# Kernel optimization log

Hardware: AMD Instinct MI355X
Metric: run time of the kernel (lower is better)

## Reference

```python
import jax, jax.numpy as jnp
import numpy as np


def setup_inputs() -> dict:
    key = jax.random.key(0)
    ks = jax.random.split(key, 10)
    V, E, H, P = 50000, 300, 512, 3
    B, S = 64, 512
    stdv = 1.0 / np.sqrt(H)
    u = lambda k, shp: jax.random.uniform(k, shp, jnp.float32, -stdv, stdv)
    return {
        "text": jax.random.randint(ks[0], (B, S), 0, V),
        "embed_table": jax.random.normal(ks[1], (V, E), jnp.float32),
        "W_z": u(ks[2], (H + E, H)),
        "b_z": u(ks[3], (H,)),
        "W_r": u(ks[4], (H + E, H)),
        "b_r": u(ks[5], (H,)),
        "W_h": u(ks[6], (H + E, H)),
        "b_h": u(ks[7], (H,)),
        "dense_W": u(ks[8], (H, P)),
        "dense_b": u(ks[9], (P,)),
    }


def reference(text, embed_table, W_z, b_z, W_r, b_r, W_h, b_h, dense_W, dense_b):
    x = embed_table[text]  # [B, S, E]
    B = x.shape[0]
    H = W_z.shape[1]
    h0 = jnp.zeros((B, H), x.dtype)
    y0 = jnp.zeros((B, H), x.dtype)

    def step(carry, x_t):
        h, _ = carry
        hx = jnp.concatenate([h, x_t], axis=1)          # [B, H+E]
        z = jax.nn.sigmoid(hx @ W_z + b_z)              # update gate
        r = jax.nn.sigmoid(hx @ W_r + b_r)              # reset gate
        y = jnp.tanh(jnp.concatenate([r * h, x_t], axis=1) @ W_h + b_h)
        h_new = (1.0 - z) * h + z * y
        return (h_new, y), None

    (h_T, y_T), _ = jax.lax.scan(step, (h0, y0), jnp.swapaxes(x, 0, 1))
    out = y_T @ dense_W + dense_b  # dense applied to last candidate y_t
    return out
```

## Files before the change

kernel.cpp:

```cpp
#include <hip/hip_runtime.h>
#include <hip/hip_bf16.h>
#include <stdint.h>

#define B_ 64
#define S_ 512
#define E_ 300
#define H_ 512
#define NG_ 1536

__global__ __launch_bounds__(256) void k_init(unsigned* __restrict__ p) {
  int i = blockIdx.x * 256 + threadIdx.x;
  if (i < 100352) p[i] = 0u;
}

__global__ __launch_bounds__(256) void k_xproj(
    const int* __restrict__ text, const float* __restrict__ emb,
    const float* __restrict__ Wz, const float* __restrict__ Wr,
    const float* __restrict__ Wh, const float* __restrict__ bz,
    const float* __restrict__ br, const float* __restrict__ bh,
    float* __restrict__ X)
{
  __shared__ float xs[32][304];
  __shared__ int   toks[32];
  const int b  = blockIdx.x >> 4;
  const int s0 = (blockIdx.x & 15) << 5;
  const int t  = threadIdx.x;

  if (t < 32) toks[t] = text[b * S_ + s0 + t];
  __syncthreads();
  for (int r = 0; r < 32; ++r) {
    const float* er = emb + (size_t)toks[r] * E_;
    for (int e = t; e < E_; e += 256) xs[r][e] = er[e];
  }
  __syncthreads();

  const int c = t & 63;
  const int q = t >> 6;
  for (int n0 = 0; n0 < NG_; n0 += 64) {
    const int n  = n0 + c;
    const int g  = n >> 9;
    const int bc = n & 511;
    const float* Wg = (g == 0) ? Wz : (g == 1) ? Wr : Wh;
    const float* bg = (g == 0) ? bz : (g == 1) ? br : bh;
    float acc[8];
    const float bias = bg[bc];
    #pragma unroll
    for (int i = 0; i < 8; ++i) acc[i] = bias;
    for (int e = 0; e < E_; e += 4) {
      const float w0 = Wg[(size_t)(H_ + e) * H_ + bc];
      const float w1 = Wg[(size_t)(H_ + e + 1) * H_ + bc];
      const float w2 = Wg[(size_t)(H_ + e + 2) * H_ + bc];
      const float w3 = Wg[(size_t)(H_ + e + 3) * H_ + bc];
      #pragma unroll
      for (int i = 0; i < 8; ++i) {
        const float4 xv = *(const float4*)&xs[(q << 3) + i][e];
        acc[i] = fmaf(xv.w, w3, fmaf(xv.z, w2, fmaf(xv.y, w1, fmaf(xv.x, w0, acc[i]))));
      }
    }
    #pragma unroll
    for (int i = 0; i < 8; ++i) {
      const int s = s0 + (q << 3) + i;
      X[((size_t)s * B_ + b) * NG_ + n] = acc[i];
    }
  }
}

__device__ __forceinline__ unsigned ld_coh_u32(const unsigned* p) {
  return __hip_atomic_load(p, __ATOMIC_RELAXED, __HIP_MEMORY_SCOPE_AGENT);
}
__device__ __forceinline__ void st_coh_u32(unsigned* p, unsigned v) {
  __hip_atomic_store(p, v, __ATOMIC_RELAXED, __HIP_MEMORY_SCOPE_AGENT);
}
__device__ __forceinline__ void st_coh_f32(float* p, float v) {
  __hip_atomic_store(p, v, __ATOMIC_RELAXED, __HIP_MEMORY_SCOPE_AGENT);
}
__device__ __forceinline__ void stage_coh(const float* src, float (*dst)[516], int t) {
  #pragma unroll
  for (int u = 0; u < 8; ++u) {
    const int e = (t << 1) + (u << 9);
    const unsigned long long v = __hip_atomic_load(
        (const unsigned long long*)(src + e), __ATOMIC_RELAXED, __HIP_MEMORY_SCOPE_AGENT);
    *(unsigned long long*)&dst[u][t << 1] = v;
  }
}

__device__ __forceinline__ void group_barrier(unsigned* gflags, unsigned* myflag,
                                              unsigned gen) {
  __syncthreads();
  const int t = threadIdx.x;
  if (t < 64) {
    if (t == 0) st_coh_u32(myflag, gen);
    unsigned v;
    int it = 0;
    do {
      v = (t < 32) ? ld_coh_u32(gflags + t * 8) : gen;
    } while (__ballot(v < gen) && ++it < 4096);
  }
  __syncthreads();
}

__global__ __launch_bounds__(256, 1) void k_gru(
    const float* __restrict__ Wz, const float* __restrict__ Wr,
    const float* __restrict__ Wh, const float* __restrict__ X,
    float* __restrict__ hb, float* __restrict__ rb,
    float* __restrict__ yb, unsigned* __restrict__ flags)
{
  __shared__ float  WT[48][516];
  __shared__ float  hs[8][516];
  __shared__ float  zs[8][16];
  __shared__ float4 pbuf[256];

  const int t = threadIdx.x;
  const int g = blockIdx.x & 7;
  const int j = blockIdx.x >> 3;
  const int colblk = j << 4;
  const int b0 = g << 3;

  float* hbuf = hb + g * (8 * H_);
  float* rbuf = rb + g * (8 * H_);
  unsigned* gflags = flags + g * 256;
  unsigned* myflag = gflags + j * 8;

  for (int idx = t; idx < 48 * 512; idx += 256) {
    const int gc = idx >> 9;
    const int k  = idx & 511;
    const float* Wsel = (gc < 16) ? Wz : (gc < 32) ? Wr : Wh;
    WT[gc][k] = Wsel[(size_t)k * H_ + colblk + (gc & 15)];
  }

  const int og  = t & 63;
  const int ksi = t >> 6;
  const int rp  = og & 3;
  const int cp  = og >> 2;
  const int ogf   = t >> 2;
  const int ef    = t & 3;
  const int rowf  = ((ogf & 3) << 1) + (ef >> 1);
  const int gcolf = ((ogf >> 2) << 1) + (ef & 1);
  const int gatef = gcolf >> 4;
  const int cf    = gcolf & 15;
  const int og2  = t & 31;
  const int ksi2 = t >> 5;
  const int rp2  = og2 & 3;
  const int cp2  = og2 >> 2;
  const int rowf2 = (((t >> 2) & 3) << 1) + ((t & 3) >> 1);
  const int cf2   = (((t >> 2) >> 2) << 1) + (t & 1);

  const float* pf = (const float*)pbuf;
  unsigned nbar = 0;
  __syncthreads();

  for (int s = 0; s < S_; ++s) {
    stage_coh(hbuf, hs, t);
    __syncthreads();

    const float* Xs = X + ((size_t)s * B_ + b0) * NG_;
    const float xv1 = Xs[rowf * NG_ + gatef * H_ + colblk + cf];
    const float xv2 = (t < 128) ? Xs[rowf2 * NG_ + 2 * H_ + colblk + cf2] : 0.f;

    {
      float p00 = 0.f, p01 = 0.f, p10 = 0.f, p11 = 0.f;
      const float* h0 = &hs[(rp << 1) + 0][0];
      const float* h1 = &hs[(rp << 1) + 1][0];
      const float* w0 = &WT[(cp << 1) + 0][0];
      const float* w1 = &WT[(cp << 1) + 1][0];
      const int k0 = ksi << 7;
      #pragma unroll 4
      for (int k = k0; k < k0 + 128; k += 4) {
        const float4 a = *(const float4*)&h0[k];
        const float4 b = *(const float4*)&h1[k];
        const float4 u = *(const float4*)&w0[k];
        const float4 v = *(const float4*)&w1[k];
        p00 = fmaf(a.x,u.x,p00); p00 = fmaf(a.y,u.y,p00); p00 = fmaf(a.z,u.z,p00); p00 = fmaf(a.w,u.w,p00);
        p01 = fmaf(a.x,v.x,p01); p01 = fmaf(a.y,v.y,p01); p01 = fmaf(a.z,v.z,p01); p01 = fmaf(a.w,v.w,p01);
        p10 = fmaf(b.x,u.x,p10); p10 = fmaf(b.y,u.y,p10); p10 = fmaf(b.z,u.z,p10); p10 = fmaf(b.w,u.w,p10);
        p11 = fmaf(b.x,v.x,p11); p11 = fmaf(b.y,v.y,p11); p11 = fmaf(b.z,v.z,p11); p11 = fmaf(b.w,v.w,p11);
      }
      pbuf[(ksi << 6) + og] = make_float4(p00, p01, p10, p11);
    }
    __syncthreads();
    {
      const float sum = pf[t] + pf[256 + t] + pf[512 + t] + pf[768 + t];
      const float pre = sum + xv1;
      const float sig = 1.f / (1.f + __expf(-pre));
      if (gatef == 0) zs[rowf][cf] = sig;
      else st_coh_f32(&rbuf[rowf * H_ + colblk + cf],
                      sig * hs[rowf][colblk + cf]);
    }

    group_barrier(gflags, myflag, ++nbar);

    float hold = 0.f, zv = 0.f;
    if (t < 128) { hold = hs[rowf2][colblk + cf2]; zv = zs[rowf2][cf2]; }
    __syncthreads();

    stage_coh(rbuf, hs, t);
    __syncthreads();

    {
      float p00 = 0.f, p01 = 0.f, p10 = 0.f, p11 = 0.f;
      const float* h0 = &hs[(rp2 << 1) + 0][0];
      const float* h1 = &hs[(rp2 << 1) + 1][0];
      const float* w0 = &WT[32 + (cp2 << 1) + 0][0];
      const float* w1 = &WT[32 + (cp2 << 1) + 1][0];
      const int k0 = ksi2 << 6;
      #pragma unroll 4
      for (int k = k0; k < k0 + 64; k += 4) {
        const float4 a = *(const float4*)&h0[k];
        const float4 b = *(const float4*)&h1[k];
        const float4 u = *(const float4*)&w0[k];
        const float4 v = *(const float4*)&w1[k];
        p00 = fmaf(a.x,u.x,p00); p00 = fmaf(a.y,u.y,p00); p00 = fmaf(a.z,u.z,p00); p00 = fmaf(a.w,u.w,p00);
        p01 = fmaf(a.x,v.x,p01); p01 = fmaf(a.y,v.y,p01); p01 = fmaf(a.z,v.z,p01); p01 = fmaf(a.w,v.w,p01);
        p10 = fmaf(b.x,u.x,p10); p10 = fmaf(b.y,u.y,p10); p10 = fmaf(b.z,u.z,p10); p10 = fmaf(b.w,u.w,p10);
        p11 = fmaf(b.x,v.x,p11); p11 = fmaf(b.y,v.y,p11); p11 = fmaf(b.z,v.z,p11); p11 = fmaf(b.w,v.w,p11);
      }
      pbuf[(ksi2 << 5) + og2] = make_float4(p00, p01, p10, p11);
    }
    __syncthreads();
    if (t < 128) {
      float sum = pf[t];
      #pragma unroll
      for (int q = 1; q < 8; ++q) sum += pf[(q << 7) + t];
      const float pre = sum + xv2;
      const float ex  = __expf(2.f * pre);
      const float y   = (ex - 1.f) / (ex + 1.f);
      const float hnew = (1.f - zv) * hold + zv * y;
      st_coh_f32(&hbuf[rowf2 * H_ + colblk + cf2], hnew);
      if (s == S_ - 1) yb[(b0 + rowf2) * H_ + colblk + cf2] = y;
    }

    group_barrier(gflags, myflag, ++nbar);
  }
}

__global__ __launch_bounds__(256) void k_dense(
    const float* __restrict__ yb, const float* __restrict__ dW,
    const float* __restrict__ db, float* __restrict__ out)
{
  const int t = threadIdx.x;
  if (t >= 192) return;
  const int b = t / 3, p = t % 3;
  float acc = db[p];
  const float* yr = yb + b * H_;
  for (int k = 0; k < H_; ++k) acc = fmaf(yr[k], dW[k * 3 + p], acc);
  out[b * 3 + p] = acc;
}

extern "C" void kernel_launch(void* const* d_in, const int* in_sizes, int n_in,
                              void* d_out, int out_size, void* d_ws, size_t ws_size,
                              hipStream_t stream) {
  const int*   text = (const int*)d_in[0];
  const float* emb  = (const float*)d_in[1];
  const float* Wz   = (const float*)d_in[2];
  const float* bz   = (const float*)d_in[3];
  const float* Wr   = (const float*)d_in[4];
  const float* br   = (const float*)d_in[5];
  const float* Wh   = (const float*)d_in[6];
  const float* bh   = (const float*)d_in[7];
  const float* dW   = (const float*)d_in[8];
  const float* db   = (const float*)d_in[9];
  float* out = (float*)d_out;

  float*    X    = (float*)d_ws;
  float*    hbp  = (float*)((char*)d_ws + (size_t)201326592);
  float*    rbp  = hbp + 32768;
  float*    ybp  = rbp + 32768;
  unsigned* flgp = (unsigned*)(ybp + 32768);

  hipLaunchKernelGGL(k_init, dim3(392), dim3(256), 0, stream, (unsigned*)hbp);

  hipLaunchKernelGGL(k_xproj, dim3(1024), dim3(256), 0, stream,
                     text, emb, Wz, Wr, Wh, bz, br, bh, X);

  const float* Wz_ = Wz; const float* Wr_ = Wr; const float* Wh_ = Wh;
  const float* X_ = X; float* hb_ = hbp; float* rb_ = rbp; float* yb_ = ybp;
  unsigned* flg_ = flgp;
  void* kargs[] = { (void*)&Wz_, (void*)&Wr_, (void*)&Wh_, (void*)&X_,
                    (void*)&hb_, (void*)&rb_, (void*)&yb_, (void*)&flg_ };
  hipLaunchCooperativeKernel((void*)k_gru, dim3(256), dim3(256), kargs, 0, stream);

  hipLaunchKernelGGL(k_dense, dim3(1), dim3(256), 0, stream, ybp, dW, db, out);
}
```

Baseline: 7.011 ms.

## Use 4x4 register tiles in GRU step GEMV and overlap barrier with prefetch

The recurrent matvec in k_gru is restructured so each thread computes a 4x4 register tile of (row, column) outputs over a k-slice. Partial sums are reduced with wave shuffles and then across waves through a smaller pbuf, which cuts LDS traffic per FMA. The group barrier is split into a flag publish and a separate poll, so the next step's X-projection loads and the hold/z reads run while other blocks arrive. The k_xproj kernel also now computes four adjacent columns per thread using float4 weight loads and stores. The cost is more registers per thread and shuffle overhead in exchange for fewer shared-memory loads and hidden sync latency.

```diff
diff --git a/kernel.cpp b/kernel.cpp
--- a/kernel.cpp
+++ b/kernel.cpp
@@ -34,33 +34,45 @@
   }
   __syncthreads();
 
-  const int c = t & 63;
-  const int q = t >> 6;
-  for (int n0 = 0; n0 < NG_; n0 += 64) {
-    const int n  = n0 + c;
+  const int c4 = t & 63;
+  const int q  = t >> 6;
+  for (int chunk = 0; chunk < 6; ++chunk) {
+    const int n  = chunk * 256 + (c4 << 2);
     const int g  = n >> 9;
     const int bc = n & 511;
     const float* Wg = (g == 0) ? Wz : (g == 1) ? Wr : Wh;
     const float* bg = (g == 0) ? bz : (g == 1) ? br : bh;
-    float acc[8];
-    const float bias = bg[bc];
-    #pragma unroll
-    for (int i = 0; i < 8; ++i) acc[i] = bias;
+    float acc[8][4];
+    {
+      const float4 bv = *(const float4*)&bg[bc];
+      #pragma unroll
+      for (int i = 0; i < 8; ++i) {
+        acc[i][0] = bv.x; acc[i][1] = bv.y; acc[i][2] = bv.z; acc[i][3] = bv.w;
+      }
+    }
     for (int e = 0; e < E_; e += 4) {
-      const float w0 = Wg[(size_t)(H_ + e) * H_ + bc];
-      const float w1 = Wg[(size_t)(H_ + e + 1) * H_ + bc];
-      const float w2 = Wg[(size_t)(H_ + e + 2) * H_ + bc];
-      const float w3 = Wg[(size_t)(H_ + e + 3) * H_ + bc];
+      float w[4][4];
+      #pragma unroll
+      for (int ee = 0; ee < 4; ++ee)
+        *(float4*)&w[ee][0] = *(const float4*)&Wg[(size_t)(H_ + e + ee) * H_ + bc];
       #pragma unroll
       for (int i = 0; i < 8; ++i) {
-        const float4 xv = *(const float4*)&xs[(q << 3) + i][e];
-        acc[i] = fmaf(xv.w, w3, fmaf(xv.z, w2, fmaf(xv.y, w1, fmaf(xv.x, w0, acc[i]))));
+        float xv[4];
+        *(float4*)xv = *(const float4*)&xs[(q << 3) + i][e];
+        #pragma unroll
+        for (int cc = 0; cc < 4; ++cc) {
+          float a = acc[i][cc];
+          #pragma unroll
+          for (int ee = 0; ee < 4; ++ee) a = fmaf(xv[ee], w[ee][cc], a);
+          acc[i][cc] = a;
+        }
       }
     }
     #pragma unroll
     for (int i = 0; i < 8; ++i) {
       const int s = s0 + (q << 3) + i;
-      X[((size_t)s * B_ + b) * NG_ + n] = acc[i];
+      *(float4*)&X[((size_t)s * B_ + b) * NG_ + n] =
+          make_float4(acc[i][0], acc[i][1], acc[i][2], acc[i][3]);
     }
   }
 }
@@ -84,19 +96,14 @@
   }
 }
 
-__device__ __forceinline__ void group_barrier(unsigned* gflags, unsigned* myflag,
-                                              unsigned gen) {
-  __syncthreads();
-  const int t = threadIdx.x;
+__device__ __forceinline__ void bar_poll(unsigned* gflags, unsigned gen, int t) {
   if (t < 64) {
-    if (t == 0) st_coh_u32(myflag, gen);
     unsigned v;
     int it = 0;
     do {
       v = (t < 32) ? ld_coh_u32(gflags + t * 8) : gen;
     } while (__ballot(v < gen) && ++it < 4096);
   }
-  __syncthreads();
 }
 
 __global__ __launch_bounds__(256, 1) void k_gru(
@@ -105,10 +112,10 @@
     float* __restrict__ hb, float* __restrict__ rb,
     float* __restrict__ yb, unsigned* __restrict__ flags)
 {
-  __shared__ float  WT[48][516];
-  __shared__ float  hs[8][516];
-  __shared__ float  zs[8][16];
-  __shared__ float4 pbuf[256];
+  __shared__ float WT[48][516];
+  __shared__ float hs[8][516];
+  __shared__ float zs[8][16];
+  __shared__ float pbuf[4][16][16];
 
   const int t = threadIdx.x;
   const int g = blockIdx.x & 7;
@@ -128,100 +135,143 @@
     WT[gc][k] = Wsel[(size_t)k * H_ + colblk + (gc & 15)];
   }
 
-  const int og  = t & 63;
-  const int ksi = t >> 6;
-  const int rp  = og & 3;
-  const int cp  = og >> 2;
-  const int ogf   = t >> 2;
-  const int ef    = t & 3;
-  const int rowf  = ((ogf & 3) << 1) + (ef >> 1);
-  const int gcolf = ((ogf >> 2) << 1) + (ef & 1);
+  const int tile1 = t & 15;
+  const int ksl1  = t >> 4;
+  const int rowf  = t >> 5;
+  const int gcolf = t & 31;
   const int gatef = gcolf >> 4;
   const int cf    = gcolf & 15;
-  const int og2  = t & 31;
-  const int ksi2 = t >> 5;
-  const int rp2  = og2 & 3;
-  const int cp2  = og2 >> 2;
-  const int rowf2 = (((t >> 2) & 3) << 1) + ((t & 3) >> 1);
-  const int cf2   = (((t >> 2) >> 2) << 1) + (t & 1);
-
-  const float* pf = (const float*)pbuf;
+  const int tilef = ((gcolf >> 2) << 1) | (rowf >> 2);
+  const int af    = ((rowf & 3) << 2) | (gcolf & 3);
+  const int tile2 = t & 7;
+  const int ksl2  = t >> 3;
+  const int rowf2  = t >> 4;
+  const int cf2    = t & 15;
+  const int tile2f = ((cf2 >> 2) << 1) | (rowf2 >> 2);
+  const int af2    = ((rowf2 & 3) << 2) | (cf2 & 3);
+
+  const int off1 = rowf * NG_ + gatef * H_ + colblk + cf;
+  const int off2 = rowf2 * NG_ + 2 * H_ + colblk + cf2;
+
   unsigned nbar = 0;
   __syncthreads();
 
+  const float* X0 = X + (size_t)b0 * NG_;
+  float xv1p = X0[off1];
+  float xv2p = (t < 128) ? X0[off2] : 0.f;
+
   for (int s = 0; s < S_; ++s) {
     stage_coh(hbuf, hs, t);
     __syncthreads();
 
-    const float* Xs = X + ((size_t)s * B_ + b0) * NG_;
-    const float xv1 = Xs[rowf * NG_ + gatef * H_ + colblk + cf];
-    const float xv2 = (t < 128) ? Xs[rowf2 * NG_ + 2 * H_ + colblk + cf2] : 0.f;
-
-    {
-      float p00 = 0.f, p01 = 0.f, p10 = 0.f, p11 = 0.f;
-      const float* h0 = &hs[(rp << 1) + 0][0];
-      const float* h1 = &hs[(rp << 1) + 1][0];
-      const float* w0 = &WT[(cp << 1) + 0][0];
-      const float* w1 = &WT[(cp << 1) + 1][0];
-      const int k0 = ksi << 7;
-      #pragma unroll 4
-      for (int k = k0; k < k0 + 128; k += 4) {
-        const float4 a = *(const float4*)&h0[k];
-        const float4 b = *(const float4*)&h1[k];
-        const float4 u = *(const float4*)&w0[k];
-        const float4 v = *(const float4*)&w1[k];
-        p00 = fmaf(a.x,u.x,p00); p00 = fmaf(a.y,u.y,p00); p00 = fmaf(a.z,u.z,p00); p00 = fmaf(a.w,u.w,p00);
-        p01 = fmaf(a.x,v.x,p01); p01 = fmaf(a.y,v.y,p01); p01 = fmaf(a.z,v.z,p01); p01 = fmaf(a.w,v.w,p01);
-        p10 = fmaf(b.x,u.x,p10); p10 = fmaf(b.y,u.y,p10); p10 = fmaf(b.z,u.z,p10); p10 = fmaf(b.w,u.w,p10);
-        p11 = fmaf(b.x,v.x,p11); p11 = fmaf(b.y,v.y,p11); p11 = fmaf(b.z,v.z,p11); p11 = fmaf(b.w,v.w,p11);
-      }
-      pbuf[(ksi << 6) + og] = make_float4(p00, p01, p10, p11);
-    }
-    __syncthreads();
-    {
-      const float sum = pf[t] + pf[256 + t] + pf[512 + t] + pf[768 + t];
-      const float pre = sum + xv1;
+    {
+      const int r0 = (tile1 & 1) << 2;
+      const int c0 = (tile1 >> 1) << 2;
+      const int k0 = ksl1 << 5;
+      float acc[16];
+      #pragma unroll
+      for (int a = 0; a < 16; ++a) acc[a] = 0.f;
+      #pragma unroll
+      for (int kk = 0; kk < 32; kk += 4) {
+        const int k = k0 + kk;
+        float4 hv[4], wv[4];
+        #pragma unroll
+        for (int ri = 0; ri < 4; ++ri) hv[ri] = *(const float4*)&hs[r0 + ri][k];
+        #pragma unroll
+        for (int ci = 0; ci < 4; ++ci) wv[ci] = *(const float4*)&WT[c0 + ci][k];
+        #pragma unroll
+        for (int ri = 0; ri < 4; ++ri)
+          #pragma unroll
+          for (int ci = 0; ci < 4; ++ci) {
+            float a = acc[(ri << 2) | ci];
+            a = fmaf(hv[ri].x, wv[ci].x, a);
+            a = fmaf(hv[ri].y, wv[ci].y, a);
+            a = fmaf(hv[ri].z, wv[ci].z, a);
+            a = fmaf(hv[ri].w, wv[ci].w, a);
+            acc[(ri << 2) | ci] = a;
+          }
+      }
+      #pragma unroll
+      for (int a = 0; a < 16; ++a) {
+        acc[a] += __shfl_xor(acc[a], 16);
+        acc[a] += __shfl_xor(acc[a], 32);
+      }
+      if ((t & 48) == 0) {
+        const int w = t >> 6;
+        #pragma unroll
+        for (int a4 = 0; a4 < 4; ++a4)
+          *(float4*)&pbuf[w][tile1][a4 << 2] =
+              make_float4(acc[a4 * 4], acc[a4 * 4 + 1], acc[a4 * 4 + 2], acc[a4 * 4 + 3]);
+      }
+    }
+    __syncthreads();
+    {
+      const float sum = pbuf[0][tilef][af] + pbuf[1][tilef][af]
+                      + pbuf[2][tilef][af] + pbuf[3][tilef][af];
+      const float pre = sum + xv1p;
       const float sig = 1.f / (1.f + __expf(-pre));
       if (gatef == 0) zs[rowf][cf] = sig;
       else st_coh_f32(&rbuf[rowf * H_ + colblk + cf],
                       sig * hs[rowf][colblk + cf]);
     }
 
-    group_barrier(gflags, myflag, ++nbar);
-
+    __syncthreads();
+    ++nbar;
+    if (t == 0) st_coh_u32(myflag, nbar);
     float hold = 0.f, zv = 0.f;
     if (t < 128) { hold = hs[rowf2][colblk + cf2]; zv = zs[rowf2][cf2]; }
+    bar_poll(gflags, nbar, t);
     __syncthreads();
 
     stage_coh(rbuf, hs, t);
     __syncthreads();
 
     {
-      float p00 = 0.f, p01 = 0.f, p10 = 0.f, p11 = 0.f;
-      const float* h0 = &hs[(rp2 << 1) + 0][0];
-      const float* h1 = &hs[(rp2 << 1) + 1][0];
-      const float* w0 = &WT[32 + (cp2 << 1) + 0][0];
-      const float* w1 = &WT[32 + (cp2 << 1) + 1][0];
-      const int k0 = ksi2 << 6;
-      #pragma unroll 4
-      for (int k = k0; k < k0 + 64; k += 4) {
-        const float4 a = *(const float4*)&h0[k];
-        const float4 b = *(const float4*)&h1[k];
-        const float4 u = *(const float4*)&w0[k];
-        const float4 v = *(const float4*)&w1[k];
-        p00 = fmaf(a.x,u.x,p00); p00 = fmaf(a.y,u.y,p00); p00 = fmaf(a.z,u.z,p00); p00 = fmaf(a.w,u.w,p00);
-        p01 = fmaf(a.x,v.x,p01); p01 = fmaf(a.y,v.y,p01); p01 = fmaf(a.z,v.z,p01); p01 = fmaf(a.w,v.w,p01);
-        p10 = fmaf(b.x,u.x,p10); p10 = fmaf(b.y,u.y,p10); p10 = fmaf(b.z,u.z,p10); p10 = fmaf(b.w,u.w,p10);
-        p11 = fmaf(b.x,v.x,p11); p11 = fmaf(b.y,v.y,p11); p11 = fmaf(b.z,v.z,p11); p11 = fmaf(b.w,v.w,p11);
-      }
-      pbuf[(ksi2 << 5) + og2] = make_float4(p00, p01, p10, p11);
+      const int r0 = (tile2 & 1) << 2;
+      const int c0 = (tile2 >> 1) << 2;
+      const int k0 = ksl2 << 4;
+      float acc[16];
+      #pragma unroll
+      for (int a = 0; a < 16; ++a) acc[a] = 0.f;
+      #pragma unroll
+      for (int kk = 0; kk < 16; kk += 4) {
+        const int k = k0 + kk;
+        float4 hv[4], wv[4];
+        #pragma unroll
+        for (int ri = 0; ri < 4; ++ri) hv[ri] = *(const float4*)&hs[r0 + ri][k];
+        #pragma unroll
+        for (int ci = 0; ci < 4; ++ci) wv[ci] = *(const float4*)&WT[32 + c0 + ci][k];
+        #pragma unroll
+        for (int ri = 0; ri < 4; ++ri)
+          #pragma unroll
+          for (int ci = 0; ci < 4; ++ci) {
+            float a = acc[(ri << 2) | ci];
+            a = fmaf(hv[ri].x, wv[ci].x, a);
+            a = fmaf(hv[ri].y, wv[ci].y, a);
+            a = fmaf(hv[ri].z, wv[ci].z, a);
+            a = fmaf(hv[ri].w, wv[ci].w, a);
+            acc[(ri << 2) | ci] = a;
+          }
+      }
+      #pragma unroll
+      for (int a = 0; a < 16; ++a) {
+        acc[a] += __shfl_xor(acc[a], 8);
+        acc[a] += __shfl_xor(acc[a], 16);
+        acc[a] += __shfl_xor(acc[a], 32);
+      }
+      if ((t & 56) == 0) {
+        const int w = t >> 6;
+        #pragma unroll
+        for (int a4 = 0; a4 < 4; ++a4)
+          *(float4*)&pbuf[w][tile2][a4 << 2] =
+              make_float4(acc[a4 * 4], acc[a4 * 4 + 1], acc[a4 * 4 + 2], acc[a4 * 4 + 3]);
+      }
     }
     __syncthreads();
     if (t < 128) {
-      float sum = pf[t];
-      #pragma unroll
-      for (int q = 1; q < 8; ++q) sum += pf[(q << 7) + t];
-      const float pre = sum + xv2;
+      const float sum = pbuf[0][tile2f][af2] + pbuf[1][tile2f][af2]
+                      + pbuf[2][tile2f][af2] + pbuf[3][tile2f][af2];
+      const float pre = sum + xv2p;
       const float ex  = __expf(2.f * pre);
       const float y   = (ex - 1.f) / (ex + 1.f);
       const float hnew = (1.f - zv) * hold + zv * y;
@@ -229,7 +279,17 @@
       if (s == S_ - 1) yb[(b0 + rowf2) * H_ + colblk + cf2] = y;
     }
 
-    group_barrier(gflags, myflag, ++nbar);
+    __syncthreads();
+    ++nbar;
+    if (t == 0) st_coh_u32(myflag, nbar);
+    {
+      const int sn = (s < S_ - 1) ? s + 1 : s;
+      const float* Xn = X + ((size_t)sn * B_ + b0) * NG_;
+      xv1p = Xn[off1];
+      if (t < 128) xv2p = Xn[off2];
+    }
+    bar_poll(gflags, nbar, t);
+    __syncthreads();
   }
 }
 
```

Measured after the change: 6.239 ms. 11.0% less time.
